# Performance work log

Hardware: AMD Instinct MI355X
Metric: run time of the kernel (lower is better)

## Reference

```python
import jax, jax.numpy as jnp
import numpy as np

B, S, D, H = 4, 2048, 1024, 16
HEAD = D // H
DENOM = float(np.sqrt(D))  # NOTE: original divides by sqrt(hidden_size), not sqrt(head_size)


def setup_inputs() -> dict:
    key = jax.random.key(0)
    ks = jax.random.split(key, 5)
    scale = 1.0 / np.sqrt(D)
    return {
        "hidden_state": jax.random.normal(ks[0], (B, S, D), dtype=jnp.float32),
        "attention_mask": jnp.ones((B, S), dtype=jnp.int32),  # unused in forward (faithful to source)
        "w_q": jax.random.normal(ks[1], (D, D), dtype=jnp.float32) * scale,
        "w_k": jax.random.normal(ks[2], (D, D), dtype=jnp.float32) * scale,
        "w_v": jax.random.normal(ks[3], (D, D), dtype=jnp.float32) * scale,
        "w_o": jax.random.normal(ks[4], (D, D), dtype=jnp.float32) * scale,
    }


def _split_heads(x):
    # [B, S, D] -> [B, H, S, head]
    b, s, _ = x.shape
    return x.reshape(b, s, H, HEAD).transpose(0, 2, 1, 3)


def reference(hidden_state, attention_mask, w_q, w_k, w_v, w_o):
    # nn.Linear(bias=False): y = x @ W^T with W of shape [out, in]
    q = _split_heads(hidden_state @ w_q.T)  # [B, H, S, head]
    k = _split_heads(hidden_state @ w_k.T)
    v = _split_heads(hidden_state @ w_v.T)
    qk = jnp.einsum("bhqd,bhkd->bhqk", q, k) / DENOM  # scale = 1/sqrt(hidden_size)
    attn = jax.nn.softmax(qk, axis=-1)  # attention_mask is NOT applied (matches source)
    ctx = jnp.einsum("bhqk,bhkd->bhqd", attn, v)  # [B, H, S, head]
    ctx = ctx.transpose(0, 2, 1, 3).reshape(hidden_state.shape[0], hidden_state.shape[1], D)
    return ctx @ w_o.T
```

## Files before the change

kernel.cpp:

```cpp
#include <hip/hip_runtime.h>
#include <hip/hip_bf16.h>
#include <math.h>

typedef __bf16 bf16x8 __attribute__((ext_vector_type(8)));
typedef __bf16 bf16x2 __attribute__((ext_vector_type(2)));
typedef float f32x4 __attribute__((ext_vector_type(4)));
typedef float f32x16 __attribute__((ext_vector_type(16)));
typedef unsigned u32x2v __attribute__((ext_vector_type(2)));
typedef unsigned u32x4v __attribute__((ext_vector_type(4)));
typedef unsigned short u16;

#define QSCALE 0.04508422002778011f

__device__ __forceinline__ u16 f2b(float f) {
  union { float f; unsigned u; } x; x.f = f;
  unsigned r = x.u + 0x7fffu + ((x.u >> 16) & 1u);
  return (u16)(r >> 16);
}

__device__ __forceinline__ unsigned pkbf(float a, float b) {
  bf16x2 t = { (__bf16)a, (__bf16)b };
  return __builtin_bit_cast(unsigned, t);
}

#define GLOAD_LDS16(g, s)                                                      \
  __builtin_amdgcn_global_load_lds(                                            \
      (__attribute__((address_space(1))) void*)(void*)(g),                     \
      (__attribute__((address_space(3))) void*)(s), 16, 0, 0)

__global__ void cast_bf16_kernel(const float* __restrict__ in, u16* __restrict__ out,
                                 int n4) {
  int i = blockIdx.x * blockDim.x + threadIdx.x;
  int stride = gridDim.x * blockDim.x;
  for (; i < n4; i += stride) {
    float4 v = ((const float4*)in)[i];
    ushort4 o;
    o.x = f2b(v.x); o.y = f2b(v.y); o.z = f2b(v.z); o.w = f2b(v.w);
    ((ushort4*)out)[i] = o;
  }
}

__global__ void cast_w4_kernel(const float* __restrict__ wq, const float* __restrict__ wk,
                               const float* __restrict__ wv, const float* __restrict__ wo,
                               u16* __restrict__ wqkv, u16* __restrict__ wob) {
  const int w = blockIdx.y;
  const float* src = (w == 0) ? wq : (w == 1) ? wk : (w == 2) ? wv : wo;
  u16* dst = (w < 3) ? wqkv + (size_t)w * 1024 * 1024 : wob;
  const float scale = (w == 0) ? QSCALE : 1.0f;
  const int n4 = 1024 * 1024 / 4;
  int i = blockIdx.x * blockDim.x + threadIdx.x;
  int stride = gridDim.x * blockDim.x;
  for (; i < n4; i += stride) {
    float4 v = ((const float4*)src)[i];
    ushort4 o;
    o.x = f2b(v.x * scale); o.y = f2b(v.y * scale);
    o.z = f2b(v.z * scale); o.w = f2b(v.w * scale);
    ((ushort4*)dst)[i] = o;
  }
}

__global__ __launch_bounds__(256) void gemm_qkv(const u16* __restrict__ A,
                                                const u16* __restrict__ Bw,
                                                u16* __restrict__ Qo,
                                                u16* __restrict__ Ko,
                                                u16* __restrict__ Vt) {
  __shared__ u16 As[128 * 32];
  __shared__ u16 Bs[128 * 32];
  const int tid = threadIdx.x;
  const int wid = tid >> 6, lane = tid & 63;
  const int fr = lane & 15, fg = lane >> 4;
  const int wr = wid >> 1, wc = wid & 1;
  const int m0 = blockIdx.y * 128, n0 = blockIdx.x * 128;
  const int K = 1024;

  f32x4 acc[4][4] = {};

  for (int kt = 0; kt < K; kt += 32) {
#pragma unroll
    for (int i2 = 0; i2 < 2; ++i2) {
      int c = i2 * 256 + tid;
      int row = c >> 2, kc = c & 3;
      GLOAD_LDS16(A + (size_t)(m0 + row) * K + kt + kc * 8, (char*)As + c * 16);
      GLOAD_LDS16(Bw + (size_t)(n0 + row) * K + kt + kc * 8, (char*)Bs + c * 16);
    }
    __syncthreads();

    bf16x8 af[4], bfr[4];
#pragma unroll
    for (int m = 0; m < 4; ++m)
      af[m] = *(const bf16x8*)((const char*)As + (wr * 64 + m * 16 + fr) * 64 + fg * 16);
#pragma unroll
    for (int n = 0; n < 4; ++n)
      bfr[n] = *(const bf16x8*)((const char*)Bs + (wc * 64 + n * 16 + fr) * 64 + fg * 16);
#pragma unroll
    for (int m = 0; m < 4; ++m)
#pragma unroll
      for (int n = 0; n < 4; ++n)
        acc[m][n] = __builtin_amdgcn_mfma_f32_16x16x32_bf16(af[m], bfr[n], acc[m][n], 0, 0, 0);
    __syncthreads();
  }

  const int region = n0 >> 10;
#pragma unroll
  for (int m = 0; m < 4; ++m)
#pragma unroll
    for (int n = 0; n < 4; ++n) {
      int gr = m0 + wr * 64 + m * 16 + fg * 4;
      int gc = n0 + wc * 64 + n * 16 + fr;
      if (region == 2) {
        int vc = gc - 2048;
        int hh = vc >> 6, d = vc & 63, bb = gr >> 11, s0 = gr & 2047;
        ushort4 o;
        o.x = f2b(acc[m][n][0]); o.y = f2b(acc[m][n][1]);
        o.z = f2b(acc[m][n][2]); o.w = f2b(acc[m][n][3]);
        *(ushort4*)(Vt + (((size_t)bb * 16 + hh) * 64 + d) * 2048 + s0) = o;
      } else {
        u16* dst = (region == 0) ? Qo : Ko;
        int cc = gc & 1023;
#pragma unroll
        for (int j = 0; j < 4; ++j)
          dst[(size_t)(gr + j) * 1024 + cc] = f2b(acc[m][n][j]);
      }
    }
}

__global__ __launch_bounds__(256) void gemm_o(const u16* __restrict__ A,
                                              const u16* __restrict__ B,
                                              float* __restrict__ Cout) {
  __shared__ u16 As[128 * 32];
  __shared__ u16 Bs[128 * 32];
  const int tid = threadIdx.x;
  const int wid = tid >> 6, lane = tid & 63;
  const int fr = lane & 15, fg = lane >> 4;
  const int wr = wid >> 1, wc = wid & 1;
  const int m0 = blockIdx.y * 128, n0 = blockIdx.x * 128;
  const int K = 1024, N = 1024;

  f32x4 acc[4][4] = {};

  for (int kt = 0; kt < K; kt += 32) {
#pragma unroll
    for (int i2 = 0; i2 < 2; ++i2) {
      int c = i2 * 256 + tid;
      int row = c >> 2, kc = c & 3;
      GLOAD_LDS16(A + (size_t)(m0 + row) * K + kt + kc * 8, (char*)As + c * 16);
      GLOAD_LDS16(B + (size_t)(n0 + row) * K + kt + kc * 8, (char*)Bs + c * 16);
    }
    __syncthreads();

    bf16x8 af[4], bfr[4];
#pragma unroll
    for (int m = 0; m < 4; ++m)
      af[m] = *(const bf16x8*)((const char*)As + (wr * 64 + m * 16 + fr) * 64 + fg * 16);
#pragma unroll
    for (int n = 0; n < 4; ++n)
      bfr[n] = *(const bf16x8*)((const char*)Bs + (wc * 64 + n * 16 + fr) * 64 + fg * 16);
#pragma unroll
    for (int m = 0; m < 4; ++m)
#pragma unroll
      for (int n = 0; n < 4; ++n)
        acc[m][n] = __builtin_amdgcn_mfma_f32_16x16x32_bf16(af[m], bfr[n], acc[m][n], 0, 0, 0);
    __syncthreads();
  }

#pragma unroll
  for (int m = 0; m < 4; ++m)
#pragma unroll
    for (int n = 0; n < 4; ++n) {
      int gr = m0 + wr * 64 + m * 16 + fg * 4;
      int gc = n0 + wc * 64 + n * 16 + fr;
#pragma unroll
      for (int j = 0; j < 4; ++j)
        Cout[(size_t)(gr + j) * N + gc] = acc[m][n][j];
    }
}

__global__ __launch_bounds__(256, 2) void attn_fwd(const u16* __restrict__ Q,
                                                   const u16* __restrict__ Kg,
                                                   const u16* __restrict__ Vtg,
                                                   u16* __restrict__ O) {
  __shared__ u16 Ks[2][64 * 64];
  __shared__ u16 Vs[2][64 * 64];
  const int tid = threadIdx.x;
  const int wid = tid >> 6, lane = tid & 63;
  const int lq = lane & 31, hi = lane >> 5;
  const int id = blockIdx.x;
  const int swz = (id & 7) * 64 + (id >> 3);
  const int qb = swz & 7, bh = swz >> 3;
  const int b = bh >> 4, h = bh & 15;
  const size_t tokBase = (size_t)b * 2048 * 1024 + h * 64;
  const size_t vBase = (size_t)bh * 64 * 2048;
  const int q0 = qb * 256 + wid * 64;

  bf16x8 qfA[4], qfB[4];
#pragma unroll
  for (int s = 0; s < 4; ++s) {
    qfA[s] = *(const bf16x8*)(Q + tokBase + (size_t)(q0 + lq) * 1024 + s * 16 + hi * 8);
    qfB[s] = *(const bf16x8*)(Q + tokBase + (size_t)(q0 + 32 + lq) * 1024 + s * 16 + hi * 8);
  }

  f32x16 accA0 = {}, accA1 = {}, accB0 = {}, accB1 = {};
  f32x16 lsvA = {}, lsvB = {};

  const int skey = tid >> 3, sdc = tid & 7;
  const int sdg = sdc ^ (skey & 7);
  const int skey2 = (tid + 256) >> 3;
  const int sdg2 = sdc ^ (skey2 & 7);

#define STAGE(bb_, k0_) do {                                                          \
    GLOAD_LDS16(Kg + tokBase + (size_t)((k0_) + skey) * 1024 + sdg * 8,               \
                (char*)Ks[bb_] + tid * 16);                                           \
    GLOAD_LDS16(Kg + tokBase + (size_t)((k0_) + skey2) * 1024 + sdg2 * 8,             \
                (char*)Ks[bb_] + (tid + 256) * 16);                                   \
    GLOAD_LDS16(Vtg + vBase + (size_t)skey * 2048 + (k0_) + sdg * 8,                  \
                (char*)Vs[bb_] + tid * 16);                                           \
    GLOAD_LDS16(Vtg + vBase + (size_t)skey2 * 2048 + (k0_) + sdg2 * 8,                \
                (char*)Vs[bb_] + (tid + 256) * 16);                                   \
  } while (0)

  STAGE(0, 0);
  for (int t = 0; t < 32; ++t) {
    const int bb = t & 1;
    __syncthreads();
    if (t < 31) STAGE(bb ^ 1, (t + 1) * 64);

    f32x16 svA0 = {}, svA1 = {}, svB0 = {}, svB1 = {};
    __builtin_amdgcn_s_setprio(1);
#pragma unroll
    for (int s = 0; s < 4; ++s) {
      bf16x8 kf0 = *(const bf16x8*)((const char*)Ks[bb] + lq * 128 +
                                    ((s * 32 + hi * 16) ^ ((lq & 7) << 4)));
      bf16x8 kf1 = *(const bf16x8*)((const char*)Ks[bb] + (32 + lq) * 128 +
                                    ((s * 32 + hi * 16) ^ ((lq & 7) << 4)));
      svA0 = __builtin_amdgcn_mfma_f32_32x32x16_bf16(kf0, qfA[s], svA0, 0, 0, 0);
      svB0 = __builtin_amdgcn_mfma_f32_32x32x16_bf16(kf0, qfB[s], svB0, 0, 0, 0);
      svA1 = __builtin_amdgcn_mfma_f32_32x32x16_bf16(kf1, qfA[s], svA1, 0, 0, 0);
      svB1 = __builtin_amdgcn_mfma_f32_32x32x16_bf16(kf1, qfB[s], svB1, 0, 0, 0);
    }
    __builtin_amdgcn_s_setprio(0);

#pragma unroll
    for (int i = 0; i < 16; ++i) svA0[i] = __builtin_amdgcn_exp2f(svA0[i]);
#pragma unroll
    for (int i = 0; i < 16; ++i) svA1[i] = __builtin_amdgcn_exp2f(svA1[i]);
#pragma unroll
    for (int i = 0; i < 16; ++i) svB0[i] = __builtin_amdgcn_exp2f(svB0[i]);
#pragma unroll
    for (int i = 0; i < 16; ++i) svB1[i] = __builtin_amdgcn_exp2f(svB1[i]);
    lsvA += svA0; lsvA += svA1;
    lsvB += svB0; lsvB += svB1;

    bf16x8 paA[4], paB[4];
#pragma unroll
    for (int kb = 0; kb < 2; ++kb) {
#pragma unroll
      for (int hh = 0; hh < 2; ++hh) {
        const int rb = hh * 8;
        {
          const f32x16& pv = kb ? svA1 : svA0;
          unsigned w01 = pkbf(pv[rb + 0], pv[rb + 1]);
          unsigned w23 = pkbf(pv[rb + 2], pv[rb + 3]);
          unsigned w45 = pkbf(pv[rb + 4], pv[rb + 5]);
          unsigned w67 = pkbf(pv[rb + 6], pv[rb + 7]);
          u32x2v ra = __builtin_amdgcn_permlane32_swap(w01, w45, false, false);
          u32x2v rc = __builtin_amdgcn_permlane32_swap(w23, w67, false, false);
          u32x4v fw = { ra[0], rc[0], ra[1], rc[1] };
          paA[kb * 2 + hh] = __builtin_bit_cast(bf16x8, fw);
        }
        {
          const f32x16& pv = kb ? svB1 : svB0;
          unsigned w01 = pkbf(pv[rb + 0], pv[rb + 1]);
          unsigned w23 = pkbf(pv[rb + 2], pv[rb + 3]);
          unsigned w45 = pkbf(pv[rb + 4], pv[rb + 5]);
          unsigned w67 = pkbf(pv[rb + 6], pv[rb + 7]);
          u32x2v ra = __builtin_amdgcn_permlane32_swap(w01, w45, false, false);
          u32x2v rc = __builtin_amdgcn_permlane32_swap(w23, w67, false, false);
          u32x4v fw = { ra[0], rc[0], ra[1], rc[1] };
          paB[kb * 2 + hh] = __builtin_bit_cast(bf16x8, fw);
        }
      }
    }

    __builtin_amdgcn_s_setprio(1);
#pragma unroll
    for (int s = 0; s < 4; ++s) {
      bf16x8 bv0 = *(const bf16x8*)((const char*)Vs[bb] + lq * 128 +
                                    ((s * 32 + hi * 16) ^ ((lq & 7) << 4)));
      bf16x8 bv1 = *(const bf16x8*)((const char*)Vs[bb] + (32 + lq) * 128 +
                                    ((s * 32 + hi * 16) ^ ((lq & 7) << 4)));
      accA0 = __builtin_amdgcn_mfma_f32_32x32x16_bf16(paA[s], bv0, accA0, 0, 0, 0);
      accA1 = __builtin_amdgcn_mfma_f32_32x32x16_bf16(paA[s], bv1, accA1, 0, 0, 0);
      accB0 = __builtin_amdgcn_mfma_f32_32x32x16_bf16(paB[s], bv0, accB0, 0, 0, 0);
      accB1 = __builtin_amdgcn_mfma_f32_32x32x16_bf16(paB[s], bv1, accB1, 0, 0, 0);
    }
    __builtin_amdgcn_s_setprio(0);
  }
#undef STAGE

  float totA = 0.f, totB = 0.f;
#pragma unroll
  for (int i = 0; i < 16; ++i) { totA += lsvA[i]; totB += lsvB[i]; }
  totA += __shfl_xor(totA, 32);
  totB += __shfl_xor(totB, 32);
  const float invA = 1.0f / totA, invB = 1.0f / totB;
#pragma unroll
  for (int r = 0; r < 16; ++r) {
    const int q = (r & 3) + 8 * (r >> 2) + 4 * hi;
    const float ivA = __shfl(invA, q);
    const float ivB = __shfl(invB, q);
    const size_t rowA = (size_t)(b * 2048 + q0 + q) * 1024 + h * 64;
    const size_t rowB = (size_t)(b * 2048 + q0 + 32 + q) * 1024 + h * 64;
    O[rowA + lq]      = f2b(accA0[r] * ivA);
    O[rowA + 32 + lq] = f2b(accA1[r] * ivA);
    O[rowB + lq]      = f2b(accB0[r] * ivB);
    O[rowB + 32 + lq] = f2b(accB1[r] * ivB);
  }
}

extern "C" void kernel_launch(void* const* d_in, const int* in_sizes, int n_in,
                              void* d_out, int out_size, void* d_ws, size_t ws_size,
                              hipStream_t stream) {
  const float* hs = (const float*)d_in[0];
  const float* wq = (const float*)d_in[2];
  const float* wk = (const float*)d_in[3];
  const float* wv = (const float*)d_in[4];
  const float* wo = (const float*)d_in[5];

  const size_t TOK = 8192, DD = 1024;
  u16* hsb  = (u16*)d_ws;
  u16* wqkv = hsb + TOK * DD;
  u16* wob  = wqkv + 3 * DD * DD;
  u16* Qb   = wob + DD * DD;
  u16* Kb   = Qb + TOK * DD;
  u16* Vtg  = Kb + TOK * DD;
  u16* Cb   = Vtg + TOK * DD;

  cast_bf16_kernel<<<2048, 256, 0, stream>>>(hs, hsb, (int)(TOK * DD / 4));
  cast_w4_kernel<<<dim3(128, 4), 256, 0, stream>>>(wq, wk, wv, wo, wqkv, wob);

  gemm_qkv<<<dim3(24, 64), 256, 0, stream>>>(hsb, wqkv, Qb, Kb, Vtg);

  attn_fwd<<<dim3(512), 256, 0, stream>>>(Qb, Kb, Vtg, Cb);

  gemm_o<<<dim3(8, 64), 256, 0, stream>>>(Cb, wob, (float*)d_out);
}
```

Measured before the change: 199.6 us.

## Load K/V fragments directly from global memory, dropping LDS double buffering

The attention kernel no longer stages K and V tiles through double-buffered shared memory with async global-to-LDS loads and barriers. Each wave now reads its K and V MFMA fragments straight from global memory into registers every iteration. Row sums are reduced to scalars inside the loop instead of in vector accumulators, which frees registers. This removes the __syncthreads and LDS traffic, but each of the four waves re-reads the same K/V tile from global memory or cache, and there is no prefetch to hide latency. The GEMM store stride is also hardcoded to 1024.

```diff
diff --git a/kernel.cpp b/kernel.cpp
--- a/kernel.cpp
+++ b/kernel.cpp
@@ -171,7 +171,7 @@
       int gc = n0 + wc * 64 + n * 16 + fr;
 #pragma unroll
       for (int j = 0; j < 4; ++j)
-        Cout[(size_t)(gr + j) * N + gc] = acc[m][n][j];
+        Cout[(size_t)(gr + j) * 1024 + gc] = acc[m][n][j];
     }
 }
 
@@ -179,8 +179,6 @@
                                                    const u16* __restrict__ Kg,
                                                    const u16* __restrict__ Vtg,
                                                    u16* __restrict__ O) {
-  __shared__ u16 Ks[2][64 * 64];
-  __shared__ u16 Vs[2][64 * 64];
   const int tid = threadIdx.x;
   const int wid = tid >> 6, lane = tid & 63;
   const int lq = lane & 31, hi = lane >> 5;
@@ -199,43 +197,38 @@
     qfB[s] = *(const bf16x8*)(Q + tokBase + (size_t)(q0 + 32 + lq) * 1024 + s * 16 + hi * 8);
   }
 
+  const u16* Kp0 = Kg + tokBase + (size_t)lq * 1024 + hi * 8;
+  const u16* Kp1 = Kg + tokBase + (size_t)(32 + lq) * 1024 + hi * 8;
+  const u16* Vp0 = Vtg + vBase + (size_t)lq * 2048 + hi * 8;
+  const u16* Vp1 = Vtg + vBase + (size_t)(32 + lq) * 2048 + hi * 8;
+
   f32x16 accA0 = {}, accA1 = {}, accB0 = {}, accB1 = {};
-  f32x16 lsvA = {}, lsvB = {};
-
-  const int skey = tid >> 3, sdc = tid & 7;
-  const int sdg = sdc ^ (skey & 7);
-  const int skey2 = (tid + 256) >> 3;
-  const int sdg2 = sdc ^ (skey2 & 7);
-
-#define STAGE(bb_, k0_) do {                                                          \
-    GLOAD_LDS16(Kg + tokBase + (size_t)((k0_) + skey) * 1024 + sdg * 8,               \
-                (char*)Ks[bb_] + tid * 16);                                           \
-    GLOAD_LDS16(Kg + tokBase + (size_t)((k0_) + skey2) * 1024 + sdg2 * 8,             \
-                (char*)Ks[bb_] + (tid + 256) * 16);                                   \
-    GLOAD_LDS16(Vtg + vBase + (size_t)skey * 2048 + (k0_) + sdg * 8,                  \
-                (char*)Vs[bb_] + tid * 16);                                           \
-    GLOAD_LDS16(Vtg + vBase + (size_t)skey2 * 2048 + (k0_) + sdg2 * 8,                \
-                (char*)Vs[bb_] + (tid + 256) * 16);                                   \
-  } while (0)
-
-  STAGE(0, 0);
+  float totA = 0.f, totB = 0.f;
+
   for (int t = 0; t < 32; ++t) {
-    const int bb = t & 1;
-    __syncthreads();
-    if (t < 31) STAGE(bb ^ 1, (t + 1) * 64);
+    const int k0 = t * 64;
+
+    bf16x8 kf0[4], kf1[4];
+#pragma unroll
+    for (int s = 0; s < 4; ++s) {
+      kf0[s] = *(const bf16x8*)(Kp0 + (size_t)k0 * 1024 + s * 16);
+      kf1[s] = *(const bf16x8*)(Kp1 + (size_t)k0 * 1024 + s * 16);
+    }
+    bf16x8 bv0[4], bv1[4];
+#pragma unroll
+    for (int s = 0; s < 4; ++s) {
+      bv0[s] = *(const bf16x8*)(Vp0 + k0 + s * 16);
+      bv1[s] = *(const bf16x8*)(Vp1 + k0 + s * 16);
+    }
 
     f32x16 svA0 = {}, svA1 = {}, svB0 = {}, svB1 = {};
     __builtin_amdgcn_s_setprio(1);
 #pragma unroll
     for (int s = 0; s < 4; ++s) {
-      bf16x8 kf0 = *(const bf16x8*)((const char*)Ks[bb] + lq * 128 +
-                                    ((s * 32 + hi * 16) ^ ((lq & 7) << 4)));
-      bf16x8 kf1 = *(const bf16x8*)((const char*)Ks[bb] + (32 + lq) * 128 +
-                                    ((s * 32 + hi * 16) ^ ((lq & 7) << 4)));
-      svA0 = __builtin_amdgcn_mfma_f32_32x32x16_bf16(kf0, qfA[s], svA0, 0, 0, 0);
-      svB0 = __builtin_amdgcn_mfma_f32_32x32x16_bf16(kf0, qfB[s], svB0, 0, 0, 0);
-      svA1 = __builtin_amdgcn_mfma_f32_32x32x16_bf16(kf1, qfA[s], svA1, 0, 0, 0);
-      svB1 = __builtin_amdgcn_mfma_f32_32x32x16_bf16(kf1, qfB[s], svB1, 0, 0, 0);
+      svA0 = __builtin_amdgcn_mfma_f32_32x32x16_bf16(kf0[s], qfA[s], svA0, 0, 0, 0);
+      svB0 = __builtin_amdgcn_mfma_f32_32x32x16_bf16(kf0[s], qfB[s], svB0, 0, 0, 0);
+      svA1 = __builtin_amdgcn_mfma_f32_32x32x16_bf16(kf1[s], qfA[s], svA1, 0, 0, 0);
+      svB1 = __builtin_amdgcn_mfma_f32_32x32x16_bf16(kf1[s], qfB[s], svB1, 0, 0, 0);
     }
     __builtin_amdgcn_s_setprio(0);
 
@@ -247,8 +240,13 @@
     for (int i = 0; i < 16; ++i) svB0[i] = __builtin_amdgcn_exp2f(svB0[i]);
 #pragma unroll
     for (int i = 0; i < 16; ++i) svB1[i] = __builtin_amdgcn_exp2f(svB1[i]);
-    lsvA += svA0; lsvA += svA1;
-    lsvB += svB0; lsvB += svB1;
+
+    {
+      float sA = 0.f, sB = 0.f;
+#pragma unroll
+      for (int i = 0; i < 16; ++i) { sA += svA0[i] + svA1[i]; sB += svB0[i] + svB1[i]; }
+      totA += sA; totB += sB;
+    }
 
     bf16x8 paA[4], paB[4];
 #pragma unroll
@@ -284,22 +282,14 @@
     __builtin_amdgcn_s_setprio(1);
 #pragma unroll
     for (int s = 0; s < 4; ++s) {
-      bf16x8 bv0 = *(const bf16x8*)((const char*)Vs[bb] + lq * 128 +
-                                    ((s * 32 + hi * 16) ^ ((lq & 7) << 4)));
-      bf16x8 bv1 = *(const bf16x8*)((const char*)Vs[bb] + (32 + lq) * 128 +
-                                    ((s * 32 + hi * 16) ^ ((lq & 7) << 4)));
-      accA0 = __builtin_amdgcn_mfma_f32_32x32x16_bf16(paA[s], bv0, accA0, 0, 0, 0);
-      accA1 = __builtin_amdgcn_mfma_f32_32x32x16_bf16(paA[s], bv1, accA1, 0, 0, 0);
-      accB0 = __builtin_amdgcn_mfma_f32_32x32x16_bf16(paB[s], bv0, accB0, 0, 0, 0);
-      accB1 = __builtin_amdgcn_mfma_f32_32x32x16_bf16(paB[s], bv1, accB1, 0, 0, 0);
+      accA0 = __builtin_amdgcn_mfma_f32_32x32x16_bf16(paA[s], bv0[s], accA0, 0, 0, 0);
+      accA1 = __builtin_amdgcn_mfma_f32_32x32x16_bf16(paA[s], bv1[s], accA1, 0, 0, 0);
+      accB0 = __builtin_amdgcn_mfma_f32_32x32x16_bf16(paB[s], bv0[s], accB0, 0, 0, 0);
+      accB1 = __builtin_amdgcn_mfma_f32_32x32x16_bf16(paB[s], bv1[s], accB1, 0, 0, 0);
     }
     __builtin_amdgcn_s_setprio(0);
   }
-#undef STAGE
-
-  float totA = 0.f, totB = 0.f;
-#pragma unroll
-  for (int i = 0; i < 16; ++i) { totA += lsvA[i]; totB += lsvB[i]; }
+
   totA += __shfl_xor(totA, 32);
   totB += __shfl_xor(totB, 32);
   const float invA = 1.0f / totA, invB = 1.0f / totB;
```

Result: slower. 256.4 us (+28.4%).
